# Performance work log

Measured on AMD Instinct MI355X. Metric: run time of the kernel, lower is better.

The kernel has to match this reference:

```python
import jax, jax.numpy as jnp
import numpy as np

B, CIN, H, W = 16, 512, 64, 64
COUT, K, LATENT = 512, 3, 512
HE_GAIN = np.sqrt(2.0)
EPS = 1e-8  # fp32 policy epsilon in the original layer


def setup_inputs() -> dict:
    key = jax.random.key(0)
    k1, k2, k3, k4 = jax.random.split(key, 4)
    return {
        "x": jax.random.normal(k1, (B, CIN, H, W), dtype=jnp.float32),
        "y": jax.random.normal(k2, (B, LATENT), dtype=jnp.float32),
        "w": jax.random.normal(k3, (K, K, CIN, COUT), dtype=jnp.float32),
        "fc_w": jax.random.normal(k4, (LATENT, CIN), dtype=jnp.float32),
        "b": jnp.zeros((CIN,), dtype=jnp.float32),
    }


def reference(x, y, w, fc_w, b):
    # Equalized-lr runtime coefficients (use_wscale=True, lrmul=1)
    runtime_coef = HE_GAIN / np.sqrt(K * K * CIN)   # conv fan_in = k*k*Cin
    fc_coef = 1.0 / np.sqrt(LATENT)                  # style FC: gain=1, fan_in=latent

    wc = w * runtime_coef                            # [K,K,Cin,Cout]
    # Style modulation: s = FC(y) + bias + 1
    s = y @ (fc_coef * fc_w) + b + 1.0               # [B,Cin]

    # Demodulation factor d[b,o] = rsqrt(sum_{k,k,c} (wc*s)^2 + eps)
    # computed without materializing the [B,K,K,Cin,Cout] modulated weight
    d = jax.lax.rsqrt(jnp.einsum('bc,hwco->bo', s * s, wc * wc) + EPS)  # [B,Cout]

    # Non-fused path: scale input per-sample, shared conv, scale output
    xm = x * s[:, :, None, None]
    out = jax.lax.conv_general_dilated(
        xm, wc, window_strides=(1, 1), padding='SAME',
        dimension_numbers=('NCHW', 'HWIO', 'NCHW'))
    return out * d[:, :, None, None]
```

## Files before the change

### kernel.cpp

```cpp
#include <hip/hip_runtime.h>
#include <hip/hip_bf16.h>
#include <stdint.h>

#define B_N   16
#define C_IN  512
#define H_    64
#define W_    64
#define C_OUT 512
#define LAT   512

#define RC      (1.0f/48.0f)
#define FC_COEF 0.044194173824159216f

typedef __attribute__((ext_vector_type(8))) short short8;
typedef __attribute__((ext_vector_type(4))) float f32x4;

typedef const void __attribute__((address_space(1))) gvoid_t;
typedef void __attribute__((address_space(3))) lvoid_t;

__device__ __forceinline__ unsigned short f2bf(float f) {
  union { float f; unsigned u; } v; v.f = f;
  unsigned r = v.u + 0x7FFFu + ((v.u >> 16) & 1u);
  return (unsigned short)(r >> 16);
}

__device__ __forceinline__ void gload_lds16(const unsigned short* g, unsigned short* l) {
  __builtin_amdgcn_global_load_lds((gvoid_t*)g, (lvoid_t*)l, 16, 0, 0);
}

__global__ void style_k(const float* __restrict__ y, const float* __restrict__ fcw,
                        const float* __restrict__ bias, float* __restrict__ s) {
  int b = blockIdx.x;
  int c = threadIdx.x;
  __shared__ float ys[LAT];
  ys[c] = y[b * LAT + c];
  __syncthreads();
  float acc = 0.f;
  for (int l = 0; l < LAT; ++l) acc += ys[l] * fcw[l * C_IN + c];
  s[b * C_IN + c] = acc * FC_COEF + bias[c] + 1.0f;
}

__global__ void wtrans_k(const float* __restrict__ w, unsigned short* __restrict__ wb,
                         float* __restrict__ t) {
  const int o0 = blockIdx.x * 64, c0 = blockIdx.y * 64;
  __shared__ unsigned short tile[64][66];
  const int tid = threadIdx.x;
  float acc[16];
#pragma unroll
  for (int i = 0; i < 16; ++i) acc[i] = 0.f;
  for (int tap = 0; tap < 9; ++tap) {
    __syncthreads();
#pragma unroll
    for (int i = 0; i < 16; ++i) {
      int row = i * 4 + (tid >> 6);
      int col = tid & 63;
      float v = w[(tap * C_IN + c0 + row) * C_OUT + o0 + col] * RC;
      acc[i] += v * v;
      tile[row][col] = f2bf(v);
    }
    __syncthreads();
#pragma unroll
    for (int i = 0; i < 16; ++i) {
      int row = i * 4 + (tid >> 6);
      int col = tid & 63;
      wb[(tap * C_OUT + o0 + row) * C_IN + c0 + col] = tile[col][row];
    }
  }
#pragma unroll
  for (int i = 0; i < 16; ++i) {
    int row = i * 4 + (tid >> 6), col = tid & 63;
    t[(c0 + row) * C_OUT + o0 + col] = acc[i];
  }
}

__global__ void demod_k(const float* __restrict__ s, const float* __restrict__ t,
                        float* __restrict__ d) {
  int b = blockIdx.x;
  int o = threadIdx.x;
  __shared__ float ss[C_IN];
  ss[o] = s[b * C_IN + o];
  __syncthreads();
  float acc = 0.f;
  for (int c = 0; c < C_IN; ++c) acc += ss[c] * ss[c] * t[c * C_OUT + o];
  d[b * C_OUT + o] = rsqrtf(acc + 1e-8f);
}

__global__ void modx_k(const float* __restrict__ x, const float* __restrict__ s,
                       unsigned short* __restrict__ xb) {
  const int h = blockIdx.x, c0 = blockIdx.y * 64, b = blockIdx.z;
  __shared__ unsigned short tile[64][66];
  const int tid = threadIdx.x;
#pragma unroll
  for (int i = 0; i < 16; ++i) {
    int row = i * 4 + (tid >> 6);
    int col = tid & 63;
    float v = x[((b * C_IN + c0 + row) * H_ + h) * W_ + col] * s[b * C_IN + c0 + row];
    tile[row][col] = f2bf(v);
  }
  __syncthreads();
#pragma unroll
  for (int i = 0; i < 16; ++i) {
    int row = i * 4 + (tid >> 6);
    int col = tid & 63;
    xb[((b * H_ + h) * W_ + row) * C_IN + c0 + col] = tile[col][row];
  }
}

__global__ __launch_bounds__(256, 3)
void conv_k(const unsigned short* __restrict__ xb,
            const unsigned short* __restrict__ wb,
            const float* __restrict__ d,
            float* __restrict__ out) {
  __shared__ __align__(16) unsigned short lds[24576];
  unsigned short* xs0 = lds;
  unsigned short* wt0 = lds + 16384;

  const int tid = threadIdx.x;
  const int pb = blockIdx.x;
  const int ob = blockIdx.y;
  const int b  = blockIdx.z;
  const int p0 = pb * 128;
  const int h0 = pb * 2;
  const int o0 = ob * 128;

  const int lane = tid & 63;
  const int wv   = tid >> 6;
  const int wm   = wv >> 1;
  const int wn   = wv & 1;
  const int kg   = lane >> 4;
  const int l16  = lane & 15;

  int a_off[4];
#pragma unroll
  for (int mf = 0; mf < 4; ++mf) {
    int m = wm * 64 + mf * 16 + l16;
    a_off[mf] = (m * 4 + (kg ^ ((m >> 1) & 3))) * 8;
  }
  int prr[4], pcc[4];
#pragma unroll
  for (int nf = 0; nf < 4; ++nf) {
    int p = wn * 64 + nf * 16 + l16;
    prr[nf] = p >> 6;
    pcc[nf] = p & 63;
  }

  const f32x4 fzero = {0.f, 0.f, 0.f, 0.f};
  const short8 szero = {0, 0, 0, 0, 0, 0, 0, 0};
  f32x4 acc[4][4];
#pragma unroll
  for (int i = 0; i < 4; ++i)
#pragma unroll
    for (int j = 0; j < 4; ++j) acc[i][j] = fzero;

  const unsigned short* xbb = xb + b * (H_ * W_ * C_IN);

  auto stage_x = [&](unsigned short* dst, int c0) {
#pragma unroll
    for (int i = 0; i < 4; ++i) {
      int col = tid >> 2, s = tid & 3;
      int g = s ^ ((col >> 1) & 3);
      int h = h0 - 1 + i;
      unsigned short* ldst = dst + (i * 256 + tid) * 8;
      if ((unsigned)h < 64u) {
        gload_lds16(xbb + ((h * 64 + col) * 512 + c0 + g * 8), ldst);
      } else {
        *(f32x4*)ldst = fzero;
      }
    }
  };
  auto stage_w = [&](unsigned short* dst, int tap, int c0) {
#pragma unroll
    for (int i = 0; i < 2; ++i) {
      int m = i * 64 + (tid >> 2), s = tid & 3;
      int g = s ^ ((m >> 1) & 3);
      gload_lds16(wb + (tap * C_OUT + o0 + m) * C_IN + c0 + g * 8,
                  dst + (i * 256 + tid) * 8);
    }
  };

  stage_x(xs0, 0);
  stage_w(wt0, 0, 0);
  __syncthreads();

  for (int chunk = 0; chunk < 16; ++chunk) {
    const int c0 = chunk * 32;
    unsigned short* xs = xs0 + (chunk & 1) * 8192;
#pragma unroll
    for (int tap = 0; tap < 9; ++tap) {
      unsigned short* wt  = wt0 + ((chunk + tap) & 1) * 4096;
      unsigned short* wtn = wt0 + (((chunk + tap) & 1) ^ 1) * 4096;
      if (tap < 8) {
        stage_w(wtn, tap + 1, c0);
      } else if (chunk + 1 < 16) {
        stage_x(xs0 + ((chunk & 1) ^ 1) * 8192, c0 + 32);
        stage_w(wtn, 0, c0 + 32);
      }
      const int kh = tap / 3;
      const int kw = tap % 3;

      short8 af[4];
#pragma unroll
      for (int mf = 0; mf < 4; ++mf)
        af[mf] = *(const short8*)(wt + a_off[mf]);

      short8 bfr[4];
#pragma unroll
      for (int nf = 0; nf < 4; ++nf) {
        int r  = prr[nf] + kh;
        int ct = pcc[nf] + kw - 1;
        bool vd = (unsigned)ct < 64u;
        int ctc = ct & 63;
        int slot = (r * 64 + ctc) * 4 + (kg ^ ((ctc >> 1) & 3));
        short8 tv = *(const short8*)(xs + slot * 8);
        bfr[nf] = vd ? tv : szero;
      }
#pragma unroll
      for (int mf = 0; mf < 4; ++mf)
#pragma unroll
        for (int nf = 0; nf < 4; ++nf)
          acc[mf][nf] = __builtin_amdgcn_mfma_f32_16x16x32_bf16(af[mf], bfr[nf], acc[mf][nf], 0, 0, 0);
      __syncthreads();
    }
  }

  const float* db = d + b * C_OUT;
  float* obase = out + (size_t)b * C_OUT * 4096;
#pragma unroll
  for (int mf = 0; mf < 4; ++mf) {
#pragma unroll
    for (int rg = 0; rg < 4; ++rg) {
      int o = o0 + wm * 64 + mf * 16 + kg * 4 + rg;
      float dv = db[o];
      float* orow = obase + (size_t)o * 4096 + p0 + wn * 64;
#pragma unroll
      for (int nf = 0; nf < 4; ++nf)
        orow[nf * 16 + l16] = acc[mf][nf][rg] * dv;
    }
  }
}

extern "C" void kernel_launch(void* const* d_in, const int* in_sizes, int n_in,
                              void* d_out, int out_size, void* d_ws, size_t ws_size,
                              hipStream_t stream) {
  const float* x    = (const float*)d_in[0];
  const float* y    = (const float*)d_in[1];
  const float* w    = (const float*)d_in[2];
  const float* fcw  = (const float*)d_in[3];
  const float* bias = (const float*)d_in[4];
  float* out = (float*)d_out;

  char* ws = (char*)d_ws;
  float* s_buf          = (float*)(ws);
  float* d_buf          = (float*)(ws + 32768);
  float* t_buf          = (float*)(ws + 65536);
  unsigned short* wbuf  = (unsigned short*)(ws + 1114112);
  unsigned short* xbuf  = (unsigned short*)(ws + 5832704);

  style_k<<<dim3(16), dim3(512), 0, stream>>>(y, fcw, bias, s_buf);
  wtrans_k<<<dim3(8, 8), dim3(256), 0, stream>>>(w, wbuf, t_buf);
  demod_k<<<dim3(16), dim3(512), 0, stream>>>(s_buf, t_buf, d_buf);
  modx_k<<<dim3(64, 8, 16), dim3(256), 0, stream>>>(x, s_buf, xbuf);
  conv_k<<<dim3(32, 4, 16), dim3(256), 0, stream>>>(xbuf, wbuf, d_buf, out);
}
```

Before: 860.1 us.

## Enlarge conv tile, triple-buffer weights, pad input halo, and parallelize style/demod

The conv kernel now uses 512 threads covering 4 output rows per block. It triple-buffers weight taps with explicit vmcnt waits and raw barriers instead of __syncthreads, and raises MFMA priority. The modulated input is written with zero halo rows so the conv staging no longer needs boundary branches. Style and demod kernels are split across more blocks, with partial sums reduced in shared memory. Together these aim to cut barrier stalls and raise load/compute overlap, at the cost of extra LDS, more register pressure, and hand-tuned wait counts that are fragile.

```diff
diff --git a/kernel.cpp b/kernel.cpp
--- a/kernel.cpp
+++ b/kernel.cpp
@@ -30,14 +30,25 @@
 
 __global__ void style_k(const float* __restrict__ y, const float* __restrict__ fcw,
                         const float* __restrict__ bias, float* __restrict__ s) {
-  int b = blockIdx.x;
-  int c = threadIdx.x;
+  const int cg = blockIdx.x, b = blockIdx.y;
+  const int tid = threadIdx.x;
+  const int cl = tid & 63, part = tid >> 6;
+  const int c = cg * 64 + cl;
   __shared__ float ys[LAT];
-  ys[c] = y[b * LAT + c];
+  __shared__ float ps[4][64];
+  ys[tid]       = y[b * LAT + tid];
+  ys[tid + 256] = y[b * LAT + tid + 256];
   __syncthreads();
   float acc = 0.f;
-  for (int l = 0; l < LAT; ++l) acc += ys[l] * fcw[l * C_IN + c];
-  s[b * C_IN + c] = acc * FC_COEF + bias[c] + 1.0f;
+  const float* fp = fcw + (part * 128) * C_IN + c;
+#pragma unroll 8
+  for (int l = 0; l < 128; ++l) acc += ys[part * 128 + l] * fp[l * C_IN];
+  ps[part][cl] = acc;
+  __syncthreads();
+  if (part == 0) {
+    float r = ps[0][cl] + ps[1][cl] + ps[2][cl] + ps[3][cl];
+    s[b * C_IN + c] = r * FC_COEF + bias[c] + 1.0f;
+  }
 }
 
 __global__ void wtrans_k(const float* __restrict__ w, unsigned short* __restrict__ wb,
@@ -75,21 +86,41 @@
 
 __global__ void demod_k(const float* __restrict__ s, const float* __restrict__ t,
                         float* __restrict__ d) {
-  int b = blockIdx.x;
-  int o = threadIdx.x;
-  __shared__ float ss[C_IN];
-  ss[o] = s[b * C_IN + o];
+  const int og = blockIdx.x, b = blockIdx.y;
+  const int tid = threadIdx.x;
+  const int ol = tid & 63, part = tid >> 6;
+  const int o = og * 64 + ol;
+  __shared__ float ssq[C_IN];
+  __shared__ float ps[4][64];
+  float v0 = s[b * C_IN + tid];       ssq[tid] = v0 * v0;
+  float v1 = s[b * C_IN + tid + 256]; ssq[tid + 256] = v1 * v1;
   __syncthreads();
   float acc = 0.f;
-  for (int c = 0; c < C_IN; ++c) acc += ss[c] * ss[c] * t[c * C_OUT + o];
-  d[b * C_OUT + o] = rsqrtf(acc + 1e-8f);
+  const float* tp = t + (part * 128) * C_OUT + o;
+#pragma unroll 8
+  for (int c = 0; c < 128; ++c) acc += ssq[part * 128 + c] * tp[c * C_OUT];
+  ps[part][ol] = acc;
+  __syncthreads();
+  if (part == 0)
+    d[b * C_OUT + o] = rsqrtf(ps[0][ol] + ps[1][ol] + ps[2][ol] + ps[3][ol] + 1e-8f);
 }
 
 __global__ void modx_k(const float* __restrict__ x, const float* __restrict__ s,
-                       unsigned short* __restrict__ xb) {
-  const int h = blockIdx.x, c0 = blockIdx.y * 64, b = blockIdx.z;
+                       unsigned short* __restrict__ xg) {
+  const int rowx = blockIdx.x;
+  const int cg = blockIdx.y, b = blockIdx.z;
+  const int c0 = cg * 64;
+  const int tid = threadIdx.x;
+  unsigned short* orow = xg + (size_t)(b * 66 + rowx) * 64 * 512;
+  if (rowx == 0 || rowx == 65) {
+    const short8 z = {0, 0, 0, 0, 0, 0, 0, 0};
+    int r = tid >> 2, q = tid & 3;
+    *(short8*)(orow + r * 512 + c0 + q * 16) = z;
+    *(short8*)(orow + r * 512 + c0 + q * 16 + 8) = z;
+    return;
+  }
+  const int h = rowx - 1;
   __shared__ unsigned short tile[64][66];
-  const int tid = threadIdx.x;
 #pragma unroll
   for (int i = 0; i < 16; ++i) {
     int row = i * 4 + (tid >> 6);
@@ -102,33 +133,34 @@
   for (int i = 0; i < 16; ++i) {
     int row = i * 4 + (tid >> 6);
     int col = tid & 63;
-    xb[((b * H_ + h) * W_ + row) * C_IN + c0 + col] = tile[col][row];
-  }
-}
-
-__global__ __launch_bounds__(256, 3)
-void conv_k(const unsigned short* __restrict__ xb,
+    orow[row * 512 + c0 + col] = tile[col][row];
+  }
+}
+
+__global__ __launch_bounds__(512, 4)
+void conv_k(const unsigned short* __restrict__ xg,
             const unsigned short* __restrict__ wb,
             const float* __restrict__ d,
             float* __restrict__ out) {
-  __shared__ __align__(16) unsigned short lds[24576];
-  unsigned short* xs0 = lds;
-  unsigned short* wt0 = lds + 16384;
-
+  __shared__ __align__(16) unsigned short lds[36864];
   const int tid = threadIdx.x;
   const int pb = blockIdx.x;
   const int ob = blockIdx.y;
   const int b  = blockIdx.z;
-  const int p0 = pb * 128;
-  const int h0 = pb * 2;
+  const int h0 = pb * 4;
+  const int p0 = pb * 256;
   const int o0 = ob * 128;
 
   const int lane = tid & 63;
   const int wv   = tid >> 6;
-  const int wm   = wv >> 1;
-  const int wn   = wv & 1;
+  const int wm   = wv >> 2;
+  const int wn   = wv & 3;
   const int kg   = lane >> 4;
   const int l16  = lane & 15;
+
+  unsigned short* const xsb0 = lds;
+  unsigned short* const xsb1 = lds + 12288;
+  unsigned short* const wsl[3] = { lds + 24576, lds + 28672, lds + 32768 };
 
   int a_off[4];
 #pragma unroll
@@ -136,13 +168,9 @@
     int m = wm * 64 + mf * 16 + l16;
     a_off[mf] = (m * 4 + (kg ^ ((m >> 1) & 3))) * 8;
   }
-  int prr[4], pcc[4];
-#pragma unroll
-  for (int nf = 0; nf < 4; ++nf) {
-    int p = wn * 64 + nf * 16 + l16;
-    prr[nf] = p >> 6;
-    pcc[nf] = p & 63;
-  }
+  int pcc[4];
+#pragma unroll
+  for (int nf = 0; nf < 4; ++nf) pcc[nf] = nf * 16 + l16;
 
   const f32x4 fzero = {0.f, 0.f, 0.f, 0.f};
   const short8 szero = {0, 0, 0, 0, 0, 0, 0, 0};
@@ -152,74 +180,62 @@
 #pragma unroll
     for (int j = 0; j < 4; ++j) acc[i][j] = fzero;
 
-  const unsigned short* xbb = xb + b * (H_ * W_ * C_IN);
+  const unsigned short* xb_b = xg + (size_t)b * 66 * 64 * 512;
 
   auto stage_x = [&](unsigned short* dst, int c0) {
 #pragma unroll
-    for (int i = 0; i < 4; ++i) {
-      int col = tid >> 2, s = tid & 3;
-      int g = s ^ ((col >> 1) & 3);
-      int h = h0 - 1 + i;
-      unsigned short* ldst = dst + (i * 256 + tid) * 8;
-      if ((unsigned)h < 64u) {
-        gload_lds16(xbb + ((h * 64 + col) * 512 + c0 + g * 8), ldst);
-      } else {
-        *(f32x4*)ldst = fzero;
-      }
+    for (int j = 0; j < 3; ++j) {
+      int lin = j * 512 + tid;
+      int r = lin >> 8, col = (lin >> 2) & 63, sx = lin & 3;
+      int g = sx ^ ((col >> 1) & 3);
+      gload_lds16(xb_b + ((h0 + r) * 64 + col) * 512 + c0 + g * 8, dst + lin * 8);
     }
   };
   auto stage_w = [&](unsigned short* dst, int tap, int c0) {
-#pragma unroll
-    for (int i = 0; i < 2; ++i) {
-      int m = i * 64 + (tid >> 2), s = tid & 3;
-      int g = s ^ ((m >> 1) & 3);
-      gload_lds16(wb + (tap * C_OUT + o0 + m) * C_IN + c0 + g * 8,
-                  dst + (i * 256 + tid) * 8);
-    }
+    int m = tid >> 2, sx = tid & 3;
+    int g = sx ^ ((m >> 1) & 3);
+    gload_lds16(wb + (tap * C_OUT + o0 + m) * C_IN + c0 + g * 8, dst + tid * 8);
   };
 
-  stage_x(xs0, 0);
-  stage_w(wt0, 0, 0);
-  __syncthreads();
+  stage_x(xsb0, 0);
+  stage_w(wsl[0], 0, 0);
+  stage_w(wsl[1], 1, 0);
 
   for (int chunk = 0; chunk < 16; ++chunk) {
-    const int c0 = chunk * 32;
-    unsigned short* xs = xs0 + (chunk & 1) * 8192;
-#pragma unroll
-    for (int tap = 0; tap < 9; ++tap) {
-      unsigned short* wt  = wt0 + ((chunk + tap) & 1) * 4096;
-      unsigned short* wtn = wt0 + (((chunk + tap) & 1) ^ 1) * 4096;
-      if (tap < 8) {
-        stage_w(wtn, tap + 1, c0);
-      } else if (chunk + 1 < 16) {
-        stage_x(xs0 + ((chunk & 1) ^ 1) * 8192, c0 + 32);
-        stage_w(wtn, 0, c0 + 32);
-      }
-      const int kh = tap / 3;
-      const int kw = tap % 3;
-
+    const int c0  = chunk * 32;
+    const int c0n = ((chunk + 1) & 15) * 32;
+    unsigned short* xs = (chunk & 1) ? xsb1 : xsb0;
+#pragma unroll
+    for (int t = 0; t < 9; ++t) {
+      if (t < 7) stage_w(wsl[(t + 2) % 3], t + 2, c0);
+      else       stage_w(wsl[(t + 2) % 3], t - 7, c0n);
+      if (t == 6) stage_x((chunk & 1) ? xsb0 : xsb1, c0n);
+      asm volatile("s_waitcnt vmcnt(%0)" :: "i"(t < 6 ? 2 : 5) : "memory");
+      __builtin_amdgcn_s_barrier();
+      __builtin_amdgcn_sched_barrier(0);
+
+      const int kh = t / 3, kw = t % 3;
+      const unsigned short* wt = wsl[t % 3];
       short8 af[4];
 #pragma unroll
       for (int mf = 0; mf < 4; ++mf)
         af[mf] = *(const short8*)(wt + a_off[mf]);
-
-      short8 bfr[4];
+      __builtin_amdgcn_s_setprio(1);
 #pragma unroll
       for (int nf = 0; nf < 4; ++nf) {
-        int r  = prr[nf] + kh;
         int ct = pcc[nf] + kw - 1;
         bool vd = (unsigned)ct < 64u;
         int ctc = ct & 63;
-        int slot = (r * 64 + ctc) * 4 + (kg ^ ((ctc >> 1) & 3));
+        int slot = ((wn + kh) * 64 + ctc) * 4 + (kg ^ ((ctc >> 1) & 3));
         short8 tv = *(const short8*)(xs + slot * 8);
-        bfr[nf] = vd ? tv : szero;
+        short8 bf = vd ? tv : szero;
+#pragma unroll
+        for (int mf = 0; mf < 4; ++mf)
+          acc[mf][nf] = __builtin_amdgcn_mfma_f32_16x16x32_bf16(af[mf], bf, acc[mf][nf], 0, 0, 0);
       }
-#pragma unroll
-      for (int mf = 0; mf < 4; ++mf)
-#pragma unroll
-        for (int nf = 0; nf < 4; ++nf)
-          acc[mf][nf] = __builtin_amdgcn_mfma_f32_16x16x32_bf16(af[mf], bfr[nf], acc[mf][nf], 0, 0, 0);
-      __syncthreads();
+      __builtin_amdgcn_s_setprio(0);
+      __builtin_amdgcn_sched_barrier(0);
+      __builtin_amdgcn_s_barrier();
     }
   }
 
@@ -254,11 +270,11 @@
   float* d_buf          = (float*)(ws + 32768);
   float* t_buf          = (float*)(ws + 65536);
   unsigned short* wbuf  = (unsigned short*)(ws + 1114112);
-  unsigned short* xbuf  = (unsigned short*)(ws + 5832704);
-
-  style_k<<<dim3(16), dim3(512), 0, stream>>>(y, fcw, bias, s_buf);
+  unsigned short* xgbuf = (unsigned short*)(ws + 5832704);
+
+  style_k<<<dim3(8, 16), dim3(256), 0, stream>>>(y, fcw, bias, s_buf);
   wtrans_k<<<dim3(8, 8), dim3(256), 0, stream>>>(w, wbuf, t_buf);
-  demod_k<<<dim3(16), dim3(512), 0, stream>>>(s_buf, t_buf, d_buf);
-  modx_k<<<dim3(64, 8, 16), dim3(256), 0, stream>>>(x, s_buf, xbuf);
-  conv_k<<<dim3(32, 4, 16), dim3(256), 0, stream>>>(xbuf, wbuf, d_buf, out);
-}
+  demod_k<<<dim3(8, 16), dim3(256), 0, stream>>>(s_buf, t_buf, d_buf);
+  modx_k<<<dim3(66, 8, 16), dim3(256), 0, stream>>>(x, s_buf, xgbuf);
+  conv_k<<<dim3(16, 4, 16), dim3(512), 0, stream>>>(xgbuf, wbuf, d_buf, out);
+}
```

Measured after the change: 762.6 us. 1.13x faster.
